# Optimization experiments

Measured on AMD Instinct MI355X. Metric: run time of the kernel, lower is better.

Reference implementation:

```python
import jax, jax.numpy as jnp
import numpy as np

D_MODEL = 1024
N_HEADS = 16
D_K = 64
D_FF = 4 * D_MODEL
LN_EPS = 1e-5


def _ln(x, g, b):
    mu = jnp.mean(x, axis=-1, keepdims=True)
    var = jnp.mean((x - mu) ** 2, axis=-1, keepdims=True)
    return (x - mu) * jax.lax.rsqrt(var + LN_EPS) * g + b


def setup_inputs() -> dict:
    key = jax.random.key(0)
    ks = jax.random.split(key, 24)
    d, h, dk, dff = D_MODEL, N_HEADS, D_K, D_FF
    s = lambda k, sh, fan: jax.random.normal(k, sh, jnp.float32) / np.sqrt(fan)
    return {
        "x": jax.random.normal(ks[0], (2, 2048, d), jnp.float32),
        "mask": jnp.ones((2, 2048), jnp.int32),
        # pre-attention q/k/v embed linears (d -> d)
        "Wqe": s(ks[1], (d, d), d), "bqe": jnp.zeros((d,), jnp.float32),
        "Wke": s(ks[2], (d, d), d), "bke": jnp.zeros((d,), jnp.float32),
        "Wve": s(ks[3], (d, d), d), "bve": jnp.zeros((d,), jnp.float32),
        # MHA projections (d -> h*dk) and output fc
        "Wq": s(ks[4], (d, h * dk), d), "bq": jnp.zeros((h * dk,), jnp.float32),
        "Wk": s(ks[5], (d, h * dk), d), "bk": jnp.zeros((h * dk,), jnp.float32),
        "Wv": s(ks[6], (d, h * dk), d), "bv": jnp.zeros((h * dk,), jnp.float32),
        "Wo": s(ks[7], (h * dk, d), h * dk), "bo": jnp.zeros((d,), jnp.float32),
        # layer norms
        "g1": jnp.ones((d,), jnp.float32), "b1": jnp.zeros((d,), jnp.float32),
        "g2": jnp.ones((d,), jnp.float32), "b2": jnp.zeros((d,), jnp.float32),
        # FFN
        "W1": s(ks[8], (d, dff), d), "bb1": jnp.zeros((dff,), jnp.float32),
        "W2": s(ks[9], (dff, d), dff), "bb2": jnp.zeros((d,), jnp.float32),
    }


def reference(x, mask, Wqe, bqe, Wke, bke, Wve, bve, Wq, bq, Wk, bk, Wv, bv,
              Wo, bo, g1, b1, g2, b2, W1, bb1, W2, bb2):
    N, T, _ = x.shape
    h, dk = N_HEADS, D_K
    # pre-embeds then MHA projections
    q = ((x @ Wqe + bqe) @ Wq + bq).reshape(N, T, h, dk)
    k = ((x @ Wke + bke) @ Wk + bk).reshape(N, T, h, dk)
    v = ((x @ Wve + bve) @ Wv + bv).reshape(N, T, h, dk)
    scores = jnp.einsum("bthd,bshd->bhts", q, k) / np.sqrt(dk).astype(np.float32)
    scores = jnp.where(mask[:, None, None, :] == 0, -jnp.inf, scores)
    attn = jax.nn.softmax(scores, axis=-1)
    a = jnp.einsum("bhts,bshd->bthd", attn, v).reshape(N, T, h * dk)
    mha_out = a @ Wo + bo
    x = _ln(x + mha_out, g1, b1)
    ffn = jax.nn.gelu(x @ W1 + bb1, approximate=False) @ W2 + bb2
    x = _ln(x + ffn, g2, b2)
    return x  # dropout is identity in eval mode
```

## Files before the change

### kernel.cpp

```cpp
#include <hip/hip_runtime.h>
#include <stdint.h>
#include <math.h>


#define DM   1024
#define DFF  4096
#define NH   16
#define DKH  64
#define TSEQ 2048
#define TOK  4096

using f32x4  = float  __attribute__((ext_vector_type(4)));
using bf16x8 = __bf16 __attribute__((ext_vector_type(8)));
using s16x8  = short  __attribute__((ext_vector_type(8)));

typedef const void __attribute__((address_space(1)))* gas_ptr;
typedef void       __attribute__((address_space(3)))* las_ptr;

__device__ __forceinline__ short f2bf(float f) {
  unsigned u; __builtin_memcpy(&u, &f, 4);
  u += 0x7FFFu + ((u >> 16) & 1u);
  return (short)(u >> 16);
}
__device__ __forceinline__ float bf2f(short s) {
  unsigned u = ((unsigned)(unsigned short)s) << 16;
  float f; __builtin_memcpy(&f, &u, 4);
  return f;
}
__device__ __forceinline__ unsigned cvt_pk_bf16(float lo, float hi) {
  unsigned r;
  asm volatile("v_cvt_pk_bf16_f32 %0, %1, %2" : "=v"(r) : "v"(lo), "v"(hi));
  return r;
}
__device__ __forceinline__ f32x4 mfma16(s16x8 a, s16x8 b, f32x4 c) {
  return __builtin_amdgcn_mfma_f32_16x16x32_bf16(
      __builtin_bit_cast(bf16x8, a), __builtin_bit_cast(bf16x8, b), c, 0, 0, 0);
}
__device__ __forceinline__ void gload16(const void* g, void* l) {
  __builtin_amdgcn_global_load_lds((gas_ptr)g, (las_ptr)l, 16, 0, 0);
}
__device__ __forceinline__ float gelu_f(float x) {
  float u = x * (0.7978845608f + 0.0356774081f * x * x);
  float e = exp2f(u * 2.8853900818f);
  return x - x / (1.f + e);
}

struct CvtArgs { const float* S[4]; short* D[4]; long n[4]; };
__global__ void cvt_bf16_b(CvtArgs a) {
  const int z = blockIdx.y;
  long i = ((long)blockIdx.x * 256 + threadIdx.x) * 8;
  if (i >= a.n[z]) return;
  const float* S = a.S[z]; short* D = a.D[z];
  float4 va = *(const float4*)(S + i);
  float4 vb = *(const float4*)(S + i + 4);
  s16x8 o;
  o[0]=f2bf(va.x); o[1]=f2bf(va.y); o[2]=f2bf(va.z); o[3]=f2bf(va.w);
  o[4]=f2bf(vb.x); o[5]=f2bf(vb.y); o[6]=f2bf(vb.z); o[7]=f2bf(vb.w);
  *(s16x8*)(D + i) = o;
}

struct TcvtArgs { const float* W[4]; short* WT[4]; };
template<int NZ>
__global__ __launch_bounds__(256) void transpose_cvt(TcvtArgs a, int R, int C) {
  __shared__ float t[64][65];
  const int z = (NZ > 1) ? blockIdx.z : 0;
  const float* __restrict__ W = a.W[z];
  short* __restrict__ WT = a.WT[z];
  const int c0 = blockIdx.x * 64, r0 = blockIdx.y * 64;
  const int tr = threadIdx.x >> 4, tc = (threadIdx.x & 15) * 4;
  #pragma unroll
  for (int q = 0; q < 4; q++) {
    int rr = q * 16 + tr;
    float4 v = *(const float4*)(W + (long)(r0 + rr) * C + c0 + tc);
    t[rr][tc] = v.x; t[rr][tc+1] = v.y; t[rr][tc+2] = v.z; t[rr][tc+3] = v.w;
  }
  __syncthreads();
  #pragma unroll
  for (int q = 0; q < 4; q++) {
    int rr = q * 16 + tr;
    short4 o;
    o.x = f2bf(t[tc+0][rr]); o.y = f2bf(t[tc+1][rr]);
    o.z = f2bf(t[tc+2][rr]); o.w = f2bf(t[tc+3][rr]);
    *(short4*)(WT + (long)(c0 + rr) * R + r0 + tc) = o;
  }
}

struct BiasArgs {
  const float* be[3]; const short* WT[3]; const float* b2[3]; float* bc[3]; int K;
};
__global__ void fuse_bias(BiasArgs a) {
  const int z = blockIdx.y, n = blockIdx.x, lane = threadIdx.x;
  const float* be = a.be[z];
  const short* WT = a.WT[z] + (long)n * a.K;
  float s = 0.f;
  for (int k = lane; k < a.K; k += 64) s += be[k] * bf2f(WT[k]);
  #pragma unroll
  for (int d = 1; d < 64; d <<= 1) s += __shfl_xor(s, d);
  if (lane == 0) a.bc[z][n] = s + a.b2[z][n];
}

struct GemmArgs {
  const short* A[3]; const short* B[3]; const float* bias[3]; void* C[6];
  float oscale[3];
  int M, N, K;
  int tmask;
  int zshift;
};

template<int EPI>
__global__ __launch_bounds__(256) void gemm_bt(GemmArgs g) {
  const int zz = blockIdx.z;
  const int prob = zz >> g.zshift;
  const int slice = zz & ((1 << g.zshift) - 1);
  const short* __restrict__ A = g.A[prob];
  const short* __restrict__ B = g.B[prob];
  const float* __restrict__ bias = g.bias[prob];
  const int N = g.N, K = g.K;
  const int Ks = K >> g.zshift;
  const int kbase = slice * Ks;
  const int tn = blockIdx.x * 128, tm = blockIdx.y * 128;
  const int tid = threadIdx.x;
  const int lane = tid & 63, w = tid >> 6;
  const int wr = w >> 1, wc = w & 1;
  const int g2 = lane >> 4, q = lane & 15;

  __shared__ alignas(16) short lbuf[2][128 * 64];
  short* lA = &lbuf[0][0];
  short* lB = &lbuf[1][0];

  f32x4 acc[4][4] = {};

  const int srow = lane >> 3;
  const int scol = lane & 7;

  for (int k0 = 0; k0 < Ks; k0 += 64) {
    #pragma unroll
    for (int qq = 0; qq < 4; qq++) {
      const int row  = w * 32 + qq * 8 + srow;
      const int slot = scol ^ (row & 7);
      gload16(A + (long)(tm + row) * K + kbase + k0 + slot * 8,
              lA + (w * 32 + qq * 8) * 64);
      gload16(B + (long)(tn + row) * K + kbase + k0 + slot * 8,
              lB + (w * 32 + qq * 8) * 64);
    }
    __syncthreads();
    #pragma unroll
    for (int kk = 0; kk < 2; kk++) {
      s16x8 af[4], bfr[4];
      #pragma unroll
      for (int m = 0; m < 4; m++) {
        const int row = wr * 64 + m * 16 + q;
        const int ps  = (kk * 4 + g2) ^ (row & 7);
        af[m] = *(const s16x8*)(lA + row * 64 + ps * 8);
      }
      #pragma unroll
      for (int n = 0; n < 4; n++) {
        const int row = wc * 64 + n * 16 + q;
        const int ps  = (kk * 4 + g2) ^ (row & 7);
        bfr[n] = *(const s16x8*)(lB + row * 64 + ps * 8);
      }
      #pragma unroll
      for (int m = 0; m < 4; m++)
        #pragma unroll
        for (int n = 0; n < 4; n++)
          acc[m][n] = mfma16(af[m], bfr[n], acc[m][n]);
    }
    __syncthreads();
  }

  const bool outT = (g.tmask >> prob) & 1;
  const float sc = g.oscale[prob];
  float bv[4];
  #pragma unroll
  for (int n = 0; n < 4; n++)
    bv[n] = bias ? bias[tn + wc * 64 + n * 16 + q] : 0.f;

  if (EPI == 1) {
    float* C = (float*)g.C[zz];
    #pragma unroll
    for (int n = 0; n < 4; n++) {
      const int col = tn + wc * 64 + n * 16 + q;
      #pragma unroll
      for (int m = 0; m < 4; m++) {
        const int row0 = tm + wr * 64 + m * 16 + g2 * 4;
        #pragma unroll
        for (int r = 0; r < 4; r++)
          C[(long)(row0 + r) * N + col] = (acc[m][n][r] + bv[n]) * sc;
      }
    }
  } else {
    short* lC = &lbuf[0][0];
    short* C = (short*)g.C[zz];
    #pragma unroll
    for (int h2 = 0; h2 < 2; h2++) {
      __syncthreads();
      if (!outT ? (wr == h2) : (wc == h2)) {
        #pragma unroll
        for (int m = 0; m < 4; m++)
          #pragma unroll
          for (int n = 0; n < 4; n++)
            #pragma unroll
            for (int r = 0; r < 4; r++) {
              float xv = (acc[m][n][r] + bv[n]) * sc;
              if (EPI == 2) xv = gelu_f(xv);
              if (!outT) {
                const int rl = m * 16 + g2 * 4 + r;
                const int cl = wc * 64 + n * 16 + q;
                lC[rl * 136 + cl] = f2bf(xv);
              } else {
                const int cl = n * 16 + q;
                const int rl = wr * 64 + m * 16 + g2 * 4 + r;
                lC[cl * 136 + rl] = f2bf(xv);
              }
            }
      }
      __syncthreads();
      const int lrow = tid >> 4, l16 = tid & 15;
      #pragma unroll
      for (int rr = 0; rr < 4; rr++) {
        const int row = rr * 16 + lrow;
        s16x8 vv = *(const s16x8*)(lC + row * 136 + l16 * 8);
        if (!outT)
          *(s16x8*)(C + (long)(tm + h2 * 64 + row) * N + tn + l16 * 8) = vv;
        else
          *(s16x8*)(C + (long)(tn + h2 * 64 + row) * g.M + tm + l16 * 8) = vv;
      }
    }
  }
}

struct Gemm256Args {
  const short* A[3]; const short* B[3]; const float* bias[3]; void* C[3];
  float oscale[3];
  int M, N, K;
  int tmask;
};

template<int EPI>
__global__ __launch_bounds__(512, 2) void gemm256(Gemm256Args g) {
  const int prob = blockIdx.z;
  const short* __restrict__ A = g.A[prob];
  const short* __restrict__ B = g.B[prob];
  const float* __restrict__ bias = g.bias[prob];
  const int N = g.N, K = g.K;

  const int gx = gridDim.x;
  const int nwg = gx * gridDim.y;
  const int bid = blockIdx.y * gx + blockIdx.x;
  const int cpx = nwg >> 3;
  const int tile = (bid & 7) * cpx + (bid >> 3);
  const int tn = (tile % gx) * 256, tm = (tile / gx) * 256;

  const int tid = threadIdx.x;
  const int lane = tid & 63, w = tid >> 6;
  const int wr = w >> 2, wc = w & 3;
  const int g2 = lane >> 4, q = lane & 15;
  const int srow = lane >> 3, scol = lane & 7;

  __shared__ alignas(16) short lA[2][256 * 64];
  __shared__ alignas(16) short lB[2][256 * 64];

  f32x4 acc[8][4] = {};

  auto STAGE = [&](int kb, int bf) {
    #pragma unroll
    for (int qq = 0; qq < 4; qq++) {
      const int row  = w * 32 + qq * 8 + srow;
      const int slot = scol ^ (row & 7);
      gload16(A + (long)(tm + row) * K + kb + slot * 8, &lA[bf][(w * 32 + qq * 8) * 64]);
      gload16(B + (long)(tn + row) * K + kb + slot * 8, &lB[bf][(w * 32 + qq * 8) * 64]);
    }
  };

  STAGE(0, 0);
  __syncthreads();

  const int nk = K >> 6;
  for (int it = 0; it < nk; it++) {
    const int cur = it & 1;
    if (it + 1 < nk) STAGE((it + 1) << 6, cur ^ 1);

    const short* cA = &lA[cur][0];
    const short* cB = &lB[cur][0];
    s16x8 bfr[4][2];
    #pragma unroll
    for (int n = 0; n < 4; n++)
      #pragma unroll
      for (int kk = 0; kk < 2; kk++) {
        const int row = wc * 64 + n * 16 + q;
        const int ps  = (kk * 4 + g2) ^ (row & 7);
        bfr[n][kk] = *(const s16x8*)(cB + row * 64 + ps * 8);
      }
    __builtin_amdgcn_s_setprio(1);
    #pragma unroll
    for (int m = 0; m < 8; m++) {
      s16x8 af[2];
      #pragma unroll
      for (int kk = 0; kk < 2; kk++) {
        const int row = wr * 128 + m * 16 + q;
        const int ps  = (kk * 4 + g2) ^ (row & 7);
        af[kk] = *(const s16x8*)(cA + row * 64 + ps * 8);
      }
      #pragma unroll
      for (int kk = 0; kk < 2; kk++)
        #pragma unroll
        for (int n = 0; n < 4; n++)
          acc[m][n] = mfma16(af[kk], bfr[n][kk], acc[m][n]);
    }
    __builtin_amdgcn_s_setprio(0);
    __syncthreads();
  }

  short* lC = &lA[0][0];
  short* C = (short*)g.C[prob];
  const bool outT = (g.tmask >> prob) & 1;
  const float sc = g.oscale[prob];
  float bv[4];
  #pragma unroll
  for (int n = 0; n < 4; n++)
    bv[n] = bias ? bias[tn + wc * 64 + n * 16 + q] : 0.f;

  #pragma unroll
  for (int p = 0; p < 4; p++) {
    __syncthreads();
    if (!outT) {
      if (wr == (p >> 1)) {
        const int mb = (p & 1) * 4;
        #pragma unroll
        for (int mm = 0; mm < 4; mm++)
          #pragma unroll
          for (int n = 0; n < 4; n++)
            #pragma unroll
            for (int r = 0; r < 4; r++) {
              float xv = (acc[mb + mm][n][r] + bv[n]) * sc;
              if (EPI == 2) xv = gelu_f(xv);
              lC[(mm * 16 + g2 * 4 + r) * 272 + wc * 64 + n * 16 + q] = f2bf(xv);
            }
      }
    } else {
      if (wc == p) {
        #pragma unroll
        for (int m = 0; m < 8; m++)
          #pragma unroll
          for (int n = 0; n < 4; n++)
            #pragma unroll
            for (int r = 0; r < 4; r++) {
              float xv = (acc[m][n][r] + bv[n]) * sc;
              lC[(n * 16 + q) * 272 + wr * 128 + m * 16 + g2 * 4 + r] = f2bf(xv);
            }
      }
    }
    __syncthreads();
    #pragma unroll
    for (int rr = 0; rr < 4; rr++) {
      const int row = rr * 16 + (tid >> 5);
      s16x8 vv = *(const s16x8*)(lC + row * 272 + (tid & 31) * 8);
      if (!outT)
        *(s16x8*)(C + (long)(tm + p * 64 + row) * N + tn + (tid & 31) * 8) = vv;
      else
        *(s16x8*)(C + (long)(tn + p * 64 + row) * g.M + tm + (tid & 31) * 8) = vv;
    }
  }
}

__global__ __launch_bounds__(256) void flash_attn(const short* __restrict__ Q,
                                                  const short* __restrict__ Km,
                                                  const short* __restrict__ VT,
                                                  const int* __restrict__ mask,
                                                  short* __restrict__ O) {
  const int qt = blockIdx.x;
  const int bh = blockIdx.y;
  const int b = bh >> 4, h = bh & 15;
  const int lane = threadIdx.x & 63, w = threadIdx.x >> 6;
  const int g2 = lane >> 4, q = lane & 15;

  __shared__ alignas(16) short lK[2][64 * 64];
  __shared__ alignas(16) short lV[2][64 * 64];
  __shared__ alignas(16) short lP[4][16 * 64];

  const int qrow0 = b * TSEQ + qt * 64 + w * 16;

  s16x8 qf[2];
  #pragma unroll
  for (int kk = 0; kk < 2; kk++)
    qf[kk] = *(const s16x8*)(Q + (long)(qrow0 + q) * DM + h * DKH + kk * 32 + g2 * 8);

  float lI = 0.f;
  f32x4 oacc[4] = {};

  const int srow = lane >> 3, scol = lane & 7;
  short* lPw = &lP[w][0];
  const int psw = (q & 7) << 3;

  const int nt = TSEQ / 64;
  #pragma unroll
  for (int t2 = 0; t2 < 2; t2++) {
    const int row  = w * 16 + t2 * 8 + srow;
    const int slot = scol ^ (row & 7);
    gload16(Km + (long)(b * TSEQ + row) * DM + h * DKH + slot * 8,
            &lK[0][(w * 16 + t2 * 8) * 64]);
    gload16(VT + (long)(h * DKH + row) * TOK + b * TSEQ + slot * 8,
            &lV[0][(w * 16 + t2 * 8) * 64]);
  }

  for (int t = 0; t < nt; t++) {
    const int cb = t & 1;
    const short* lKc = &lK[cb][0];
    const short* lVc = &lV[cb][0];
    __syncthreads();

    if (t + 1 < nt) {
      const int kvn = (t + 1) * 64;
      #pragma unroll
      for (int t2 = 0; t2 < 2; t2++) {
        const int row  = w * 16 + t2 * 8 + srow;
        const int slot = scol ^ (row & 7);
        gload16(Km + (long)(b * TSEQ + kvn + row) * DM + h * DKH + slot * 8,
                &lK[cb ^ 1][(w * 16 + t2 * 8) * 64]);
        gload16(VT + (long)(h * DKH + row) * TOK + b * TSEQ + kvn + slot * 8,
                &lV[cb ^ 1][(w * 16 + t2 * 8) * 64]);
      }
    }
    const int mk = mask[b * TSEQ + t * 64 + lane];

    f32x4 s[4] = {};
    __builtin_amdgcn_s_setprio(1);
    #pragma unroll
    for (int kk = 0; kk < 2; kk++)
      #pragma unroll
      for (int n = 0; n < 4; n++) {
        const int row = n * 16 + q;
        const int ps  = (kk * 4 + g2) ^ (row & 7);
        s16x8 kf = *(const s16x8*)(lKc + row * 64 + ps * 8);
        s[n] = mfma16(kf, qf[kk], s[n]);
      }
    __builtin_amdgcn_s_setprio(0);

    float p[4][4];
    #pragma unroll
    for (int n = 0; n < 4; n++)
      #pragma unroll
      for (int r = 0; r < 4; r++)
        p[n][r] = exp2f(s[n][r]);

    if (__ballot(mk == 0)) {
      const float mzf = mk ? 1.f : 0.f;
      #pragma unroll
      for (int n = 0; n < 4; n++)
        #pragma unroll
        for (int r = 0; r < 4; r++)
          p[n][r] *= __shfl(mzf, n * 16 + g2 * 4 + r);
    }
    #pragma unroll
    for (int n = 0; n < 4; n++)
      lI += (p[n][0] + p[n][1]) + (p[n][2] + p[n][3]);

    #pragma unroll
    for (int n = 0; n < 4; n++)
      #pragma unroll
      for (int hh = 0; hh < 2; hh++) {
        unsigned pk = cvt_pk_bf16(p[n][2 * hh], p[n][2 * hh + 1]);
        *(unsigned*)(lPw + ((q * 64 + n * 16 + g2 * 4 + 2 * hh) ^ psw)) = pk;
      }
    s16x8 pf[2];
    #pragma unroll
    for (int kk = 0; kk < 2; kk++)
      pf[kk] = *(const s16x8*)(lPw + ((q * 64 + kk * 32 + g2 * 8) ^ psw));

    __builtin_amdgcn_s_setprio(1);
    #pragma unroll
    for (int kk = 0; kk < 2; kk++)
      #pragma unroll
      for (int n = 0; n < 4; n++) {
        const int row = n * 16 + q;
        const int ps  = (kk * 4 + g2) ^ (row & 7);
        s16x8 vf = *(const s16x8*)(lVc + row * 64 + ps * 8);
        oacc[n] = mfma16(pf[kk], vf, oacc[n]);
      }
    __builtin_amdgcn_s_setprio(0);
  }

  lI += __shfl_xor(lI, 16);
  lI += __shfl_xor(lI, 32);
  float rI[4];
  #pragma unroll
  for (int r = 0; r < 4; r++) rI[r] = 1.f / __shfl(lI, g2 * 4 + r);
  #pragma unroll
  for (int n = 0; n < 4; n++) {
    const int col = h * DKH + n * 16 + q;
    #pragma unroll
    for (int r = 0; r < 4; r++) {
      const int row = qrow0 + g2 * 4 + r;
      O[(long)row * DM + col] = f2bf(oacc[n][r] * rI[r]);
    }
  }
}

template<bool WB16>
__global__ __launch_bounds__(256) void ln_residual(const float* __restrict__ X,
                                                   const float* __restrict__ P0,
                                                   const float* __restrict__ P1,
                                                   const float* __restrict__ rbias,
                                                   const float* __restrict__ gw,
                                                   const float* __restrict__ bw,
                                                   float* __restrict__ Yf,
                                                   short* __restrict__ Yb) {
  const int row = blockIdx.x, tid = threadIdx.x;
  const float4 xv = *(const float4*)(X + (long)row * DM + tid * 4);
  const float4 p0 = *(const float4*)(P0 + (long)row * DM + tid * 4);
  const float4 p1 = *(const float4*)(P1 + (long)row * DM + tid * 4);
  const float4 rb = *(const float4*)(rbias + tid * 4);
  float v[4] = {xv.x + p0.x + p1.x + rb.x, xv.y + p0.y + p1.y + rb.y,
                xv.z + p0.z + p1.z + rb.z, xv.w + p0.w + p1.w + rb.w};
  float s  = v[0] + v[1] + v[2] + v[3];
  float s2 = v[0]*v[0] + v[1]*v[1] + v[2]*v[2] + v[3]*v[3];
  #pragma unroll
  for (int d = 1; d < 64; d <<= 1) { s += __shfl_xor(s, d); s2 += __shfl_xor(s2, d); }
  __shared__ float red[8];
  const int lane = tid & 63, w = tid >> 6;
  if (lane == 0) { red[w] = s; red[w + 4] = s2; }
  __syncthreads();
  s  = red[0] + red[1] + red[2] + red[3];
  s2 = red[4] + red[5] + red[6] + red[7];
  const float mu  = s * (1.f / DM);
  const float inv = rsqrtf(s2 * (1.f / DM) - mu * mu + 1e-5f);
  #pragma unroll
  for (int i = 0; i < 4; i++) {
    const int col = tid * 4 + i;
    const float y = (v[i] - mu) * inv * gw[col] + bw[col];
    Yf[(long)row * DM + col] = y;
    if (WB16) Yb[(long)row * DM + col] = f2bf(y);
  }
}

extern "C" void kernel_launch(void* const* d_in, const int* in_sizes, int n_in,
                              void* d_out, int out_size, void* d_ws, size_t ws_size,
                              hipStream_t stream) {
  const float* x   = (const float*)d_in[0];
  const int*   msk = (const int*)d_in[1];
  const float* Wqe = (const float*)d_in[2];  const float* bqe = (const float*)d_in[3];
  const float* Wke = (const float*)d_in[4];  const float* bke = (const float*)d_in[5];
  const float* Wve = (const float*)d_in[6];  const float* bve = (const float*)d_in[7];
  const float* Wq  = (const float*)d_in[8];  const float* bq  = (const float*)d_in[9];
  const float* Wk  = (const float*)d_in[10]; const float* bk  = (const float*)d_in[11];
  const float* Wv  = (const float*)d_in[12]; const float* bv  = (const float*)d_in[13];
  const float* Wo  = (const float*)d_in[14]; const float* bo  = (const float*)d_in[15];
  const float* g1  = (const float*)d_in[16]; const float* b1  = (const float*)d_in[17];
  const float* g2  = (const float*)d_in[18]; const float* b2  = (const float*)d_in[19];
  const float* W1  = (const float*)d_in[20]; const float* bb1 = (const float*)d_in[21];
  const float* W2  = (const float*)d_in[22]; const float* bb2 = (const float*)d_in[23];

  char* ws = (char*)d_ws;
  const size_t MB = 1024ull * 1024ull;
  short* xb   = (short*)(ws + 0);
  short* woT  = (short*)(ws + 8 * MB);
  short* w1T  = (short*)(ws + 10 * MB);
  short* w2T  = (short*)(ws + 18 * MB);
  short* wqeB = (short*)(ws + 26 * MB);
  short* wkeB = (short*)(ws + 28 * MB);
  short* wveB = (short*)(ws + 30 * MB);
  short* wqT  = (short*)(ws + 32 * MB);
  short* wkT  = (short*)(ws + 34 * MB);
  short* wvT  = (short*)(ws + 36 * MB);
  short* wcqT = (short*)(ws + 38 * MB);
  short* wckT = (short*)(ws + 40 * MB);
  short* wcvT = (short*)(ws + 42 * MB);
  float* bcq  = (float*)(ws + 44 * MB);
  float* bck  = (float*)(ws + 44 * MB + 16384);
  float* bcv  = (float*)(ws + 44 * MB + 32768);
  short* Qb   = (short*)(ws + 45 * MB);
  short* Kb2  = (short*)(ws + 53 * MB);
  short* VTb  = (short*)(ws + 61 * MB);
  float* mhaP0= (float*)(ws + 26 * MB);
  float* mhaP1= (float*)(ws + 42 * MB);
  short* Hb   = (short*)(ws + 26 * MB);
  float* yf   = (float*)(ws + 58 * MB);
  short* ybf  = (short*)(ws + 74 * MB);
  float* ffnP0= (float*)d_out;
  float* ffnP1= (float*)(ws + 0);
  short* Aout = xb;

  CvtArgs ca = {};
  ca.S[0] = x;  ca.D[0] = xb;   ca.n[0] = (long)TOK * DM;
  ca.S[1] = Wqe; ca.D[1] = wqeB; ca.n[1] = (long)DM * DM;
  ca.S[2] = Wke; ca.D[2] = wkeB; ca.n[2] = (long)DM * DM;
  ca.S[3] = Wve; ca.D[3] = wveB; ca.n[3] = (long)DM * DM;
  cvt_bf16_b<<<dim3((long)TOK * DM / 2048, 4), 256, 0, stream>>>(ca);

  TcvtArgs t4 = {};
  t4.W[0] = Wq; t4.WT[0] = wqT;  t4.W[1] = Wk; t4.WT[1] = wkT;
  t4.W[2] = Wv; t4.WT[2] = wvT;  t4.W[3] = Wo; t4.WT[3] = woT;
  transpose_cvt<4><<<dim3(16, 16, 4), 256, 0, stream>>>(t4, DM, DM);
  TcvtArgs t1 = {}; t1.W[0] = W1; t1.WT[0] = w1T;
  transpose_cvt<1><<<dim3(64, 16), 256, 0, stream>>>(t1, DM, DFF);
  TcvtArgs t2 = {}; t2.W[0] = W2; t2.WT[0] = w2T;
  transpose_cvt<1><<<dim3(16, 64), 256, 0, stream>>>(t2, DFF, DM);

  GemmArgs fa = {};
  fa.A[0] = wqT;  fa.A[1] = wkT;  fa.A[2] = wvT;
  fa.B[0] = wqeB; fa.B[1] = wkeB; fa.B[2] = wveB;
  fa.C[0] = wcqT; fa.C[1] = wckT; fa.C[2] = wcvT;
  fa.oscale[0] = 1.f; fa.oscale[1] = 1.f; fa.oscale[2] = 1.f;
  fa.M = DM; fa.N = DM; fa.K = DM; fa.tmask = 0; fa.zshift = 0;
  gemm_bt<0><<<dim3(8, 8, 3), 256, 0, stream>>>(fa);

  BiasArgs ba = {};
  ba.be[0] = bqe; ba.be[1] = bke; ba.be[2] = bve;
  ba.WT[0] = wqT; ba.WT[1] = wkT; ba.WT[2] = wvT;
  ba.b2[0] = bq;  ba.b2[1] = bk;  ba.b2[2] = bv;
  ba.bc[0] = bcq; ba.bc[1] = bck; ba.bc[2] = bcv; ba.K = DM;
  fuse_bias<<<dim3(DM, 3), 64, 0, stream>>>(ba);

  Gemm256Args qa = {};
  qa.A[0] = xb;   qa.A[1] = xb;   qa.A[2] = xb;
  qa.B[0] = wcqT; qa.B[1] = wckT; qa.B[2] = wcvT;
  qa.bias[0] = bcq; qa.bias[1] = bck; qa.bias[2] = bcv;
  qa.C[0] = Qb; qa.C[1] = Kb2; qa.C[2] = VTb;
  qa.oscale[0] = 0.125f * 1.44269504f; qa.oscale[1] = 1.f; qa.oscale[2] = 1.f;
  qa.M = TOK; qa.N = DM; qa.K = DM; qa.tmask = 4;
  gemm256<0><<<dim3(4, 16, 3), 512, 0, stream>>>(qa);

  flash_attn<<<dim3(TSEQ / 64, 2 * NH), 256, 0, stream>>>(Qb, Kb2, VTb, msk, Aout);

  GemmArgs oa = {};
  oa.A[0] = Aout; oa.B[0] = woT; oa.bias[0] = nullptr;
  oa.C[0] = mhaP0; oa.C[1] = mhaP1;
  oa.oscale[0] = 1.f;
  oa.M = TOK; oa.N = DM; oa.K = DM; oa.tmask = 0; oa.zshift = 1;
  gemm_bt<1><<<dim3(8, 32, 2), 256, 0, stream>>>(oa);

  ln_residual<true><<<dim3(TOK), 256, 0, stream>>>(x, mhaP0, mhaP1, bo,
                                                   g1, b1, yf, ybf);

  Gemm256Args f1 = {};
  f1.A[0] = ybf; f1.B[0] = w1T; f1.bias[0] = bb1; f1.C[0] = Hb;
  f1.oscale[0] = 1.f;
  f1.M = TOK; f1.N = DFF; f1.K = DM; f1.tmask = 0;
  gemm256<2><<<dim3(16, 16, 1), 512, 0, stream>>>(f1);

  GemmArgs f2 = {};
  f2.A[0] = Hb; f2.B[0] = w2T; f2.bias[0] = nullptr;
  f2.C[0] = ffnP0; f2.C[1] = ffnP1;
  f2.oscale[0] = 1.f;
  f2.M = TOK; f2.N = DM; f2.K = DFF; f2.tmask = 0; f2.zshift = 1;
  gemm_bt<1><<<dim3(8, 32, 2), 256, 0, stream>>>(f2);

  ln_residual<false><<<dim3(TOK), 256, 0, stream>>>(yf, ffnP0, ffnP1, bb2,
                                                    g2, b2, (float*)d_out, nullptr);
}
```

Measured before the change: 309.8 us.

## Process two query sub-tiles per wave in attention and compute row sums with MFMA

Each wave in the attention kernel now handles 32 query rows instead of 16, so every K and V fragment read from LDS feeds two MFMAs. The block's query tile doubles to 128 and the grid halves. The softmax denominator now comes from an MFMA of the bf16 probabilities against a ones vector, replacing the scalar accumulation and cross-lane shuffles. This raises register pressure, halves the block count (512 blocks) and uses the bf16-rounded probabilities for the denominator.

```diff
diff --git a/kernel.cpp b/kernel.cpp
--- a/kernel.cpp
+++ b/kernel.cpp
@@ -371,36 +371,43 @@
   const int qt = blockIdx.x;
   const int bh = blockIdx.y;
   const int b = bh >> 4, h = bh & 15;
-  const int lane = threadIdx.x & 63, w = threadIdx.x >> 6;
+  const int tid = threadIdx.x;
+  const int lane = tid & 63, w = tid >> 6;
   const int g2 = lane >> 4, q = lane & 15;
 
   __shared__ alignas(16) short lK[2][64 * 64];
   __shared__ alignas(16) short lV[2][64 * 64];
-  __shared__ alignas(16) short lP[4][16 * 64];
-
-  const int qrow0 = b * TSEQ + qt * 64 + w * 16;
-
-  s16x8 qf[2];
-  #pragma unroll
-  for (int kk = 0; kk < 2; kk++)
-    qf[kk] = *(const s16x8*)(Q + (long)(qrow0 + q) * DM + h * DKH + kk * 32 + g2 * 8);
-
-  float lI = 0.f;
-  f32x4 oacc[4] = {};
+  __shared__ alignas(16) short lP[4][2][16 * 64];
+
+  const int qrow0 = b * TSEQ + qt * 128 + w * 32;
+
+  s16x8 qf0[2], qf1[2];
+  #pragma unroll
+  for (int kk = 0; kk < 2; kk++) {
+    qf0[kk] = *(const s16x8*)(Q + (long)(qrow0 + q) * DM + h * DKH + kk * 32 + g2 * 8);
+    qf1[kk] = *(const s16x8*)(Q + (long)(qrow0 + 16 + q) * DM + h * DKH + kk * 32 + g2 * 8);
+  }
+
+  f32x4 oacc0[4] = {}, oacc1[4] = {};
+  f32x4 dacc0 = {}, dacc1 = {};
+  s16x8 vones;
+  #pragma unroll
+  for (int j = 0; j < 8; j++) vones[j] = (short)0x3F80;
 
   const int srow = lane >> 3, scol = lane & 7;
-  short* lPw = &lP[w][0];
+  short* lP0 = &lP[w][0][0];
+  short* lP1 = &lP[w][1][0];
   const int psw = (q & 7) << 3;
 
   const int nt = TSEQ / 64;
   #pragma unroll
-  for (int t2 = 0; t2 < 2; t2++) {
-    const int row  = w * 16 + t2 * 8 + srow;
+  for (int c = 0; c < 2; c++) {
+    const int row = w * 16 + c * 8 + srow;
     const int slot = scol ^ (row & 7);
     gload16(Km + (long)(b * TSEQ + row) * DM + h * DKH + slot * 8,
-            &lK[0][(w * 16 + t2 * 8) * 64]);
+            &lK[0][(w * 16 + c * 8) * 64]);
     gload16(VT + (long)(h * DKH + row) * TOK + b * TSEQ + slot * 8,
-            &lV[0][(w * 16 + t2 * 8) * 64]);
+            &lV[0][(w * 16 + c * 8) * 64]);
   }
 
   for (int t = 0; t < nt; t++) {
@@ -412,18 +419,18 @@
     if (t + 1 < nt) {
       const int kvn = (t + 1) * 64;
       #pragma unroll
-      for (int t2 = 0; t2 < 2; t2++) {
-        const int row  = w * 16 + t2 * 8 + srow;
+      for (int c = 0; c < 2; c++) {
+        const int row = w * 16 + c * 8 + srow;
         const int slot = scol ^ (row & 7);
         gload16(Km + (long)(b * TSEQ + kvn + row) * DM + h * DKH + slot * 8,
-                &lK[cb ^ 1][(w * 16 + t2 * 8) * 64]);
+                &lK[cb ^ 1][(w * 16 + c * 8) * 64]);
         gload16(VT + (long)(h * DKH + row) * TOK + b * TSEQ + kvn + slot * 8,
-                &lV[cb ^ 1][(w * 16 + t2 * 8) * 64]);
+                &lV[cb ^ 1][(w * 16 + c * 8) * 64]);
       }
     }
     const int mk = mask[b * TSEQ + t * 64 + lane];
 
-    f32x4 s[4] = {};
+    f32x4 s0[4] = {}, s1[4] = {};
     __builtin_amdgcn_s_setprio(1);
     #pragma unroll
     for (int kk = 0; kk < 2; kk++)
@@ -432,66 +439,76 @@
         const int row = n * 16 + q;
         const int ps  = (kk * 4 + g2) ^ (row & 7);
         s16x8 kf = *(const s16x8*)(lKc + row * 64 + ps * 8);
-        s[n] = mfma16(kf, qf[kk], s[n]);
+        s0[n] = mfma16(kf, qf0[kk], s0[n]);
+        s1[n] = mfma16(kf, qf1[kk], s1[n]);
       }
     __builtin_amdgcn_s_setprio(0);
 
-    float p[4][4];
+    float p0[4][4], p1[4][4];
     #pragma unroll
     for (int n = 0; n < 4; n++)
       #pragma unroll
-      for (int r = 0; r < 4; r++)
-        p[n][r] = exp2f(s[n][r]);
+      for (int r = 0; r < 4; r++) {
+        p0[n][r] = exp2f(s0[n][r]);
+        p1[n][r] = exp2f(s1[n][r]);
+      }
 
     if (__ballot(mk == 0)) {
       const float mzf = mk ? 1.f : 0.f;
       #pragma unroll
       for (int n = 0; n < 4; n++)
         #pragma unroll
-        for (int r = 0; r < 4; r++)
-          p[n][r] *= __shfl(mzf, n * 16 + g2 * 4 + r);
-    }
+        for (int r = 0; r < 4; r++) {
+          const float mm2 = __shfl(mzf, n * 16 + g2 * 4 + r);
+          p0[n][r] *= mm2;
+          p1[n][r] *= mm2;
+        }
+    }
+
     #pragma unroll
     for (int n = 0; n < 4; n++)
-      lI += (p[n][0] + p[n][1]) + (p[n][2] + p[n][3]);
-
-    #pragma unroll
-    for (int n = 0; n < 4; n++)
       #pragma unroll
       for (int hh = 0; hh < 2; hh++) {
-        unsigned pk = cvt_pk_bf16(p[n][2 * hh], p[n][2 * hh + 1]);
-        *(unsigned*)(lPw + ((q * 64 + n * 16 + g2 * 4 + 2 * hh) ^ psw)) = pk;
-      }
-    s16x8 pf[2];
-    #pragma unroll
-    for (int kk = 0; kk < 2; kk++)
-      pf[kk] = *(const s16x8*)(lPw + ((q * 64 + kk * 32 + g2 * 8) ^ psw));
+        const int off = (q * 64 + n * 16 + g2 * 4 + 2 * hh) ^ psw;
+        *(unsigned*)(lP0 + off) = cvt_pk_bf16(p0[n][2 * hh], p0[n][2 * hh + 1]);
+        *(unsigned*)(lP1 + off) = cvt_pk_bf16(p1[n][2 * hh], p1[n][2 * hh + 1]);
+      }
+    s16x8 pf0[2], pf1[2];
+    #pragma unroll
+    for (int kk = 0; kk < 2; kk++) {
+      const int off = (q * 64 + kk * 32 + g2 * 8) ^ psw;
+      pf0[kk] = *(const s16x8*)(lP0 + off);
+      pf1[kk] = *(const s16x8*)(lP1 + off);
+    }
 
     __builtin_amdgcn_s_setprio(1);
     #pragma unroll
-    for (int kk = 0; kk < 2; kk++)
+    for (int kk = 0; kk < 2; kk++) {
       #pragma unroll
       for (int n = 0; n < 4; n++) {
         const int row = n * 16 + q;
         const int ps  = (kk * 4 + g2) ^ (row & 7);
         s16x8 vf = *(const s16x8*)(lVc + row * 64 + ps * 8);
-        oacc[n] = mfma16(pf[kk], vf, oacc[n]);
-      }
+        oacc0[n] = mfma16(pf0[kk], vf, oacc0[n]);
+        oacc1[n] = mfma16(pf1[kk], vf, oacc1[n]);
+      }
+      dacc0 = mfma16(pf0[kk], vones, dacc0);
+      dacc1 = mfma16(pf1[kk], vones, dacc1);
+    }
     __builtin_amdgcn_s_setprio(0);
   }
 
-  lI += __shfl_xor(lI, 16);
-  lI += __shfl_xor(lI, 32);
-  float rI[4];
-  #pragma unroll
-  for (int r = 0; r < 4; r++) rI[r] = 1.f / __shfl(lI, g2 * 4 + r);
+  float rI0[4], rI1[4];
+  #pragma unroll
+  for (int r = 0; r < 4; r++) { rI0[r] = 1.f / dacc0[r]; rI1[r] = 1.f / dacc1[r]; }
   #pragma unroll
   for (int n = 0; n < 4; n++) {
     const int col = h * DKH + n * 16 + q;
     #pragma unroll
     for (int r = 0; r < 4; r++) {
-      const int row = qrow0 + g2 * 4 + r;
-      O[(long)row * DM + col] = f2bf(oacc[n][r] * rI[r]);
+      const int row0 = qrow0 + g2 * 4 + r;
+      O[(long)row0 * DM + col] = f2bf(oacc0[n][r] * rI0[r]);
+      O[(long)(row0 + 16) * DM + col] = f2bf(oacc1[n][r] * rI1[r]);
     }
   }
 }
@@ -620,7 +637,7 @@
   qa.M = TOK; qa.N = DM; qa.K = DM; qa.tmask = 4;
   gemm256<0><<<dim3(4, 16, 3), 512, 0, stream>>>(qa);
 
-  flash_attn<<<dim3(TSEQ / 64, 2 * NH), 256, 0, stream>>>(Qb, Kb2, VTb, msk, Aout);
+  flash_attn<<<dim3(TSEQ / 128, 2 * NH), 256, 0, stream>>>(Qb, Kb2, VTb, msk, Aout);
 
   GemmArgs oa = {};
   oa.A[0] = Aout; oa.B[0] = woT; oa.bias[0] = nullptr;
```

Measured after the change: 309.8 us. About the same (+0.0%).
